# Kernel tuning notes

Measured on AMD Instinct MI355X. Metric: run time of the kernel, lower is better.

Reference implementation:

```python
import jax, jax.numpy as jnp
import numpy as np

N = 100000   # nodes
E = 1600000  # edges (avg degree 16)
D = 128      # in_channels == out_channels
L2_EPS = 1e-12   # F.normalize eps
GN_EPS = 1e-5    # GraphNorm eps


def setup_inputs() -> dict:
    key = jax.random.key(0)
    ks = jax.random.split(key, 6)
    x = jax.random.normal(ks[0], (N, D), dtype=jnp.float32)
    edge_index = jax.random.randint(ks[1], (2, E), 0, N, dtype=jnp.int32)
    batch = jnp.zeros((N,), dtype=jnp.int32)  # single graph
    scale = 1.0 / np.sqrt(D)
    Wl = jax.random.normal(ks[2], (D, D), dtype=jnp.float32) * scale  # SAGE lin_l (neighbor), has bias
    bl = jnp.zeros((D,), dtype=jnp.float32)
    Wr = jax.random.normal(ks[3], (D, D), dtype=jnp.float32) * scale  # SAGE lin_r (root), no bias
    gn_weight = jnp.ones((D,), dtype=jnp.float32)       # GraphNorm gamma
    gn_bias = jnp.zeros((D,), dtype=jnp.float32)        # GraphNorm beta
    gn_mean_scale = jnp.ones((D,), dtype=jnp.float32)   # GraphNorm alpha
    return {"x": x, "edge_index": edge_index, "batch": batch,
            "Wl": Wl, "bl": bl, "Wr": Wr,
            "gn_weight": gn_weight, "gn_bias": gn_bias, "gn_mean_scale": gn_mean_scale}


def reference(x, edge_index, batch, Wl, bl, Wr, gn_weight, gn_bias, gn_mean_scale):
    src, dst = edge_index[0], edge_index[1]
    n = x.shape[0]
    # ---- SAGEConv (aggr='mean', normalize=True) ----
    deg = jax.ops.segment_sum(jnp.ones(src.shape[0], x.dtype), dst, num_segments=n)
    agg = jax.ops.segment_sum(x[src], dst, num_segments=n)  # gather -> scatter-add [N, D]
    agg = agg / jnp.maximum(deg, 1.0)[:, None]              # mean aggregation
    h = agg @ Wl.T + bl + x @ Wr.T                          # lin_l(agg) + lin_r(x)
    h = h / jnp.maximum(jnp.linalg.norm(h, axis=-1, keepdims=True), L2_EPS)  # row L2 norm
    # ---- GraphNorm (batch is all zeros -> single graph stats) ----
    mean = jnp.mean(h, axis=0, keepdims=True)               # [1, D]
    centered = h - gn_mean_scale * mean
    var = jnp.mean(centered * centered, axis=0, keepdims=True)
    h = gn_weight * centered / jnp.sqrt(var + GN_EPS) + gn_bias
    # ---- activation (exact GELU, as torch nn.GELU) + dropout(eval=identity) + residual ----
    h = jax.nn.gelu(h, approximate=False)
    return h + x
```

## Files before the change

### kernel.cpp

```cpp
#include <hip/hip_runtime.h>
#include <cstdint>

#define DF 128

typedef float f32x4 __attribute__((ext_vector_type(4)));
typedef short bf16x8 __attribute__((ext_vector_type(8)));

__device__ __forceinline__ unsigned short f2bf(float f) {
  unsigned int u = __float_as_uint(f);
  return (unsigned short)((u + 0x7fffu + ((u >> 16) & 1u)) >> 16);
}
__device__ __forceinline__ unsigned int pack2(float lo, float hi) {
  return (unsigned int)f2bf(lo) | ((unsigned int)f2bf(hi) << 16);
}
__device__ __forceinline__ float bflo(unsigned int u) { return __uint_as_float(u << 16); }
__device__ __forceinline__ float bfhi(unsigned int u) { return __uint_as_float(u & 0xffff0000u); }

__global__ void k_wcvt(const float* __restrict__ Wl, const float* __restrict__ Wr,
                       unsigned short* __restrict__ wbf) {
  int i = blockIdx.x * 256 + threadIdx.x;
  int c = i >> 8;
  int k = i & 255;
  float v = (k < DF) ? Wl[c * DF + k] : Wr[c * DF + (k - DF)];
  wbf[i] = f2bf(v);
}

__global__ void k_xcvt(const float* __restrict__ x, unsigned int* __restrict__ xbf, int total8) {
  int i = blockIdx.x * 256 + threadIdx.x;
  if (i >= total8) return;
  const float4* xr = (const float4*)(x + (size_t)i * 8);
  float4 a = xr[0], b = xr[1];
  uint4 v;
  v.x = pack2(a.x, a.y);
  v.y = pack2(a.z, a.w);
  v.z = pack2(b.x, b.y);
  v.w = pack2(b.z, b.w);
  ((uint4*)xbf)[i] = v;
}

__global__ void k_deg(const int* __restrict__ ei, int* __restrict__ deg, int E) {
  int e = blockIdx.x * 256 + threadIdx.x;
  if (e < E) atomicAdd(&deg[ei[(size_t)E + e]], 1);
}

__global__ void k_off(const int* __restrict__ deg, int* __restrict__ start,
                      int* __restrict__ cursor, int* __restrict__ total, int n) {
  int i = blockIdx.x * 256 + threadIdx.x;
  if (i < n) {
    int d = deg[i];
    int p = atomicAdd(total, d);
    start[i] = p;
    cursor[i] = p;
  }
}

__global__ void k_fill(const int* __restrict__ ei, int* __restrict__ cursor,
                       int* __restrict__ adj, int E) {
  int e = blockIdx.x * 256 + threadIdx.x;
  if (e < E) {
    int s = ei[e];
    int t = ei[(size_t)E + e];
    int p = atomicAdd(&cursor[t], 1);
    adj[p] = s;
  }
}

template <int BF>
__global__ void k_agg(const float* __restrict__ xf, const unsigned int* __restrict__ xb,
                      const int* __restrict__ start, const int* __restrict__ deg,
                      const int* __restrict__ adj, unsigned short* __restrict__ aggbf, int n) {
  int node = blockIdx.x * 4 + (threadIdx.x >> 6);
  if (node >= n) return;
  int lane = threadIdx.x & 63;
  int rs = start[node];
  int d = deg[node];
  float s0 = 0.f, s1 = 0.f;
  int j = 0;
  for (; j + 4 <= d; j += 4) {
    int i0 = adj[rs + j], i1 = adj[rs + j + 1], i2 = adj[rs + j + 2], i3 = adj[rs + j + 3];
    if (BF) {
      unsigned int u0 = xb[(size_t)i0 * 64 + lane], u1 = xb[(size_t)i1 * 64 + lane],
                   u2 = xb[(size_t)i2 * 64 + lane], u3 = xb[(size_t)i3 * 64 + lane];
      s0 += bflo(u0) + bflo(u1) + bflo(u2) + bflo(u3);
      s1 += bfhi(u0) + bfhi(u1) + bfhi(u2) + bfhi(u3);
    } else {
      const float2* x2 = (const float2*)xf;
      float2 v0 = x2[(size_t)i0 * 64 + lane], v1 = x2[(size_t)i1 * 64 + lane],
             v2 = x2[(size_t)i2 * 64 + lane], v3 = x2[(size_t)i3 * 64 + lane];
      s0 += v0.x + v1.x + v2.x + v3.x;
      s1 += v0.y + v1.y + v2.y + v3.y;
    }
  }
  for (; j < d; ++j) {
    int i0 = adj[rs + j];
    if (BF) {
      unsigned int u0 = xb[(size_t)i0 * 64 + lane];
      s0 += bflo(u0);
      s1 += bfhi(u0);
    } else {
      const float2* x2 = (const float2*)xf;
      float2 v = x2[(size_t)i0 * 64 + lane];
      s0 += v.x;
      s1 += v.y;
    }
  }
  float inv = 1.0f / (float)(d > 1 ? d : 1);
  *(unsigned int*)(aggbf + (size_t)node * DF + lane * 2) = pack2(s0 * inv, s1 * inv);
}

template <int XBF>
__global__ __launch_bounds__(256) void k_gemm(
    const unsigned short* __restrict__ aggbf, const unsigned short* __restrict__ xbf,
    const float* __restrict__ x, const unsigned short* __restrict__ wbf,
    const float* __restrict__ bl, float* __restrict__ hout,
    float* __restrict__ pf, int n) {
  __shared__ __align__(16) unsigned short Abuf[64 * 128];
  __shared__ __align__(16) unsigned short Bbuf[128 * 128];
  int tid = threadIdx.x;
  int node0 = blockIdx.x * 64;
  int wv = tid >> 6, lane = tid & 63;
  int lo = lane & 15, hi = lane >> 4;

  f32x4 acc[8] = {};

  int arow = wv * 16 + lo;
  int abase = arow * 256 + hi * 16;
  int aswz = (arow & 7) << 4;

  for (int ph = 0; ph < 2; ++ph) {
    if (ph) __syncthreads();
    if (ph == 0 || XBF) {
      const unsigned short* src = ph == 0 ? aggbf : xbf;
#pragma unroll
      for (int it = 0; it < 4; ++it) {
        int id = it * 256 + tid;
        int row = id >> 4;
        int inner = (id & 15) * 16;
        uint4 v = make_uint4(0u, 0u, 0u, 0u);
        int gr = node0 + row;
        if (gr < n) v = *(const uint4*)(src + (size_t)gr * DF + inner / 2);
        *(uint4*)((char*)Abuf + ((row * 256 + inner) ^ ((row & 7) << 4))) = v;
      }
    } else {
#pragma unroll
      for (int it = 0; it < 4; ++it) {
        int id = it * 256 + tid;
        int row = id >> 4;
        int inner = (id & 15) * 16;
        int e0 = inner / 2;
        uint4 v = make_uint4(0u, 0u, 0u, 0u);
        int gr = node0 + row;
        if (gr < n) {
          const float4* xr = (const float4*)(x + (size_t)gr * DF + e0);
          float4 a = xr[0], b = xr[1];
          v.x = pack2(a.x, a.y);
          v.y = pack2(a.z, a.w);
          v.z = pack2(b.x, b.y);
          v.w = pack2(b.z, b.w);
        }
        *(uint4*)((char*)Abuf + ((row * 256 + inner) ^ ((row & 7) << 4))) = v;
      }
    }
#pragma unroll
    for (int it = 0; it < 8; ++it) {
      int id = it * 256 + tid;
      int c = id >> 4;
      int inner = (id & 15) * 16;
      uint4 v = *(const uint4*)((const char*)wbf + (size_t)c * 512 + ph * 256 + inner);
      *(uint4*)((char*)Bbuf + ((c * 256 + inner) ^ ((c & 7) << 4))) = v;
    }
    __syncthreads();
#pragma unroll
    for (int kk = 0; kk < 4; ++kk) {
      bf16x8 af = *(const bf16x8*)((const char*)Abuf + ((abase + kk * 64) ^ aswz));
#pragma unroll
      for (int f = 0; f < 8; ++f) {
        int brow = f * 16 + lo;
        int bb = (brow * 256 + hi * 16 + kk * 64) ^ ((brow & 7) << 4);
        bf16x8 bfr = *(const bf16x8*)((const char*)Bbuf + bb);
        acc[f] = __builtin_amdgcn_mfma_f32_16x16x32_bf16(af, bfr, acc[f], 0, 0, 0);
      }
    }
  }

  int r0 = node0 + wv * 16 + hi * 4;
#pragma unroll
  for (int f = 0; f < 8; ++f) {
    float b = bl[f * 16 + lo];
#pragma unroll
    for (int r = 0; r < 4; ++r) acc[f][r] += b;
  }
#pragma unroll
  for (int r = 0; r < 4; ++r) {
    if (r0 + r >= n) {
#pragma unroll
      for (int f = 0; f < 8; ++f) acc[f][r] = 0.f;
    }
  }
  float ss[4] = {0.f, 0.f, 0.f, 0.f};
#pragma unroll
  for (int f = 0; f < 8; ++f)
#pragma unroll
    for (int r = 0; r < 4; ++r) ss[r] += acc[f][r] * acc[f][r];
#pragma unroll
  for (int m = 1; m <= 8; m <<= 1) {
#pragma unroll
    for (int r = 0; r < 4; ++r) ss[r] += __shfl_xor(ss[r], m, 64);
  }
#pragma unroll
  for (int r = 0; r < 4; ++r) {
    float inv = 1.0f / fmaxf(sqrtf(ss[r]), 1e-12f);
#pragma unroll
    for (int f = 0; f < 8; ++f) acc[f][r] *= inv;
  }
  float s1[8], s2[8];
#pragma unroll
  for (int f = 0; f < 8; ++f) { s1[f] = 0.f; s2[f] = 0.f; }
#pragma unroll
  for (int f = 0; f < 8; ++f) {
#pragma unroll
    for (int r = 0; r < 4; ++r) {
      float v = acc[f][r];
      s1[f] += v;
      s2[f] += v * v;
      if (r0 + r < n) hout[(size_t)(r0 + r) * DF + f * 16 + lo] = v;
    }
  }
#pragma unroll
  for (int f = 0; f < 8; ++f) {
    s1[f] += __shfl_xor(s1[f], 16, 64);
    s1[f] += __shfl_xor(s1[f], 32, 64);
    s2[f] += __shfl_xor(s2[f], 16, 64);
    s2[f] += __shfl_xor(s2[f], 32, 64);
  }
  __syncthreads();
  float* red = (float*)Abuf;
  if (hi == 0) {
#pragma unroll
    for (int f = 0; f < 8; ++f) {
      red[wv * 256 + f * 16 + lo] = s1[f];
      red[wv * 256 + 128 + f * 16 + lo] = s2[f];
    }
  }
  __syncthreads();
  float v = red[tid] + red[256 + tid] + red[512 + tid] + red[768 + tid];
  pf[(size_t)blockIdx.x * 256 + tid] = v;
}

__global__ void k_reduce(const float* __restrict__ pf, float* __restrict__ pf2, int NB) {
  int g = blockIdx.x, t = threadIdx.x;
  int L = (NB + 15) / 16;
  int b0 = g * L, b1 = (b0 + L < NB) ? b0 + L : NB;
  float a = 0.f;
  for (int r = b0; r < b1; ++r) a += pf[(size_t)r * 256 + t];
  pf2[g * 256 + t] = a;
}

__global__ void k_coef(const float* __restrict__ pf2,
                       const float* __restrict__ gnw, const float* __restrict__ gnb,
                       const float* __restrict__ alpha, float* __restrict__ coef, int n) {
  int j = threadIdx.x;
  float s = 0.f, q = 0.f;
#pragma unroll
  for (int g = 0; g < 16; ++g) {
    s += pf2[g * 256 + j];
    q += pf2[g * 256 + 128 + j];
  }
  float invn = 1.0f / (float)n;
  float mean = s * invn;
  float m2 = q * invn;
  float a = alpha[j];
  float var = m2 - mean * mean * (2.0f * a - a * a);
  float ca = gnw[j] / sqrtf(var + 1e-5f);
  float cb = gnb[j] - ca * a * mean;
  coef[j] = ca;
  coef[DF + j] = cb;
}

__global__ void k_final(float* __restrict__ out, const float* __restrict__ x,
                        const float* __restrict__ coef, int total4) {
  int i = blockIdx.x * 256 + threadIdx.x;
  if (i >= total4) return;
  int cj = (i & 31) * 4;
  float4 h = ((const float4*)out)[i];
  float4 xv = ((const float4*)x)[i];
  float4 ca = *(const float4*)(coef + cj);
  float4 cb = *(const float4*)(coef + DF + cj);
  float4 o;
#define GEL(comp)                                                         \
  {                                                                       \
    float v = ca.comp * h.comp + cb.comp;                                 \
    float g = 0.5f * v * (1.0f + erff(v * 0.70710678118654752f));         \
    o.comp = g + xv.comp;                                                 \
  }
  GEL(x) GEL(y) GEL(z) GEL(w)
#undef GEL
  ((float4*)out)[i] = o;
}

extern "C" void kernel_launch(void* const* d_in, const int* in_sizes, int n_in,
                              void* d_out, int out_size, void* d_ws, size_t ws_size,
                              hipStream_t stream) {
  const float* x = (const float*)d_in[0];
  const int* ei = (const int*)d_in[1];
  const float* Wl = (const float*)d_in[3];
  const float* bl = (const float*)d_in[4];
  const float* Wr = (const float*)d_in[5];
  const float* gnw = (const float*)d_in[6];
  const float* gnb = (const float*)d_in[7];
  const float* alpha = (const float*)d_in[8];
  int n = in_sizes[2];
  int E = in_sizes[1] / 2;
  int NB = (n + 63) / 64;
  float* out = (float*)d_out;
  (void)n_in; (void)out_size;

  char* ws = (char*)d_ws;
  int* deg = (int*)ws;
  int* total = (int*)(ws + (size_t)n * 4);
  size_t zbytes = (size_t)(n + 1) * 4;
  size_t off = (zbytes + 255) & ~(size_t)255;
  auto carve = [&](size_t b) {
    char* p = ws + off;
    off = (off + b + 255) & ~(size_t)255;
    return p;
  };
  int* start = (int*)carve((size_t)n * 4);
  int* cursor = (int*)carve((size_t)n * 4);
  int* adjv = (int*)carve((size_t)E * 4);
  unsigned short* wbf = (unsigned short*)carve((size_t)DF * 256 * 2);
  float* coef = (float*)carve(256 * 4);
  float* pf = (float*)carve((size_t)NB * 256 * 4);
  float* pf2 = (float*)carve(16 * 256 * 4);
  unsigned short* aggbf = (unsigned short*)carve((size_t)n * DF * 2);
  size_t need_bf = off + (size_t)n * DF * 2;
  int useBF = (ws_size >= need_bf) ? 1 : 0;
  unsigned int* xbf = (unsigned int*)carve((size_t)n * DF * 2);

  hipMemsetAsync(ws, 0, zbytes, stream);
  k_wcvt<<<(DF * 256) / 256, 256, 0, stream>>>(Wl, Wr, wbf);
  k_deg<<<(E + 255) / 256, 256, 0, stream>>>(ei, deg, E);
  k_off<<<(n + 255) / 256, 256, 0, stream>>>(deg, start, cursor, total, n);
  k_fill<<<(E + 255) / 256, 256, 0, stream>>>(ei, cursor, adjv, E);
  if (useBF) {
    k_xcvt<<<(n * 16 + 255) / 256, 256, 0, stream>>>(x, xbf, n * 16);
    k_agg<1><<<(n + 3) / 4, 256, 0, stream>>>(x, xbf, start, deg, adjv, aggbf, n);
    k_gemm<1><<<NB, 256, 0, stream>>>(aggbf, (const unsigned short*)xbf, x, wbf, bl, out, pf, n);
  } else {
    k_agg<0><<<(n + 3) / 4, 256, 0, stream>>>(x, xbf, start, deg, adjv, aggbf, n);
    k_gemm<0><<<NB, 256, 0, stream>>>(aggbf, (const unsigned short*)xbf, x, wbf, bl, out, pf, n);
  }
  k_reduce<<<16, 256, 0, stream>>>(pf, pf2, NB);
  k_coef<<<1, DF, 0, stream>>>(pf2, gnw, gnb, alpha, coef, n);
  k_final<<<(n * (DF / 4) + 255) / 256, 256, 0, stream>>>(out, x, coef, n * (DF / 4));
}
```

Measured before the change: 470.7 us.

## Bucket edges by 64-node tile and fuse aggregation into GEMM via LDS atomics

Replaces the per-node CSR build (global atomics for degree, offset and fill) with a deterministic block histogram, scan and scatter that buckets edges by destination tile of 64 nodes, packing source and local destination into one word. The GEMM kernel then aggregates its tile's neighbours itself, accumulating in shared memory with float atomics, computing degrees locally, and writing bf16 A tiles straight to LDS. This removes the separate aggregation kernel and the global round trip of the aggregated matrix. In exchange it relies on heavy LDS atomic traffic and larger shared memory per block, which may lower occupancy. Summation order also becomes nondeterministic.

```diff
diff --git a/kernel.cpp b/kernel.cpp
--- a/kernel.cpp
+++ b/kernel.cpp
@@ -38,99 +38,205 @@
   ((uint4*)xbf)[i] = v;
 }
 
-__global__ void k_deg(const int* __restrict__ ei, int* __restrict__ deg, int E) {
-  int e = blockIdx.x * 256 + threadIdx.x;
-  if (e < E) atomicAdd(&deg[ei[(size_t)E + e]], 1);
-}
-
-__global__ void k_off(const int* __restrict__ deg, int* __restrict__ start,
-                      int* __restrict__ cursor, int* __restrict__ total, int n) {
-  int i = blockIdx.x * 256 + threadIdx.x;
-  if (i < n) {
-    int d = deg[i];
-    int p = atomicAdd(total, d);
-    start[i] = p;
-    cursor[i] = p;
-  }
-}
-
-__global__ void k_fill(const int* __restrict__ ei, int* __restrict__ cursor,
-                       int* __restrict__ adj, int E) {
-  int e = blockIdx.x * 256 + threadIdx.x;
-  if (e < E) {
-    int s = ei[e];
-    int t = ei[(size_t)E + e];
-    int p = atomicAdd(&cursor[t], 1);
-    adj[p] = s;
-  }
-}
-
-template <int BF>
-__global__ void k_agg(const float* __restrict__ xf, const unsigned int* __restrict__ xb,
-                      const int* __restrict__ start, const int* __restrict__ deg,
-                      const int* __restrict__ adj, unsigned short* __restrict__ aggbf, int n) {
-  int node = blockIdx.x * 4 + (threadIdx.x >> 6);
-  if (node >= n) return;
-  int lane = threadIdx.x & 63;
-  int rs = start[node];
-  int d = deg[node];
-  float s0 = 0.f, s1 = 0.f;
-  int j = 0;
-  for (; j + 4 <= d; j += 4) {
-    int i0 = adj[rs + j], i1 = adj[rs + j + 1], i2 = adj[rs + j + 2], i3 = adj[rs + j + 3];
-    if (BF) {
-      unsigned int u0 = xb[(size_t)i0 * 64 + lane], u1 = xb[(size_t)i1 * 64 + lane],
-                   u2 = xb[(size_t)i2 * 64 + lane], u3 = xb[(size_t)i3 * 64 + lane];
-      s0 += bflo(u0) + bflo(u1) + bflo(u2) + bflo(u3);
-      s1 += bfhi(u0) + bfhi(u1) + bfhi(u2) + bfhi(u3);
-    } else {
-      const float2* x2 = (const float2*)xf;
-      float2 v0 = x2[(size_t)i0 * 64 + lane], v1 = x2[(size_t)i1 * 64 + lane],
-             v2 = x2[(size_t)i2 * 64 + lane], v3 = x2[(size_t)i3 * 64 + lane];
-      s0 += v0.x + v1.x + v2.x + v3.x;
-      s1 += v0.y + v1.y + v2.y + v3.y;
-    }
-  }
-  for (; j < d; ++j) {
-    int i0 = adj[rs + j];
-    if (BF) {
-      unsigned int u0 = xb[(size_t)i0 * 64 + lane];
-      s0 += bflo(u0);
-      s1 += bfhi(u0);
-    } else {
-      const float2* x2 = (const float2*)xf;
-      float2 v = x2[(size_t)i0 * 64 + lane];
-      s0 += v.x;
-      s1 += v.y;
-    }
-  }
-  float inv = 1.0f / (float)(d > 1 ? d : 1);
-  *(unsigned int*)(aggbf + (size_t)node * DF + lane * 2) = pack2(s0 * inv, s1 * inv);
+__global__ __launch_bounds__(256) void k_hist(const int* __restrict__ ei,
+                                              unsigned int* __restrict__ hist,
+                                              int E, int NBK, int CE) {
+  __shared__ unsigned int h[4096];
+  for (int i = threadIdx.x; i < NBK; i += 256) h[i] = 0u;
+  __syncthreads();
+  int b0 = blockIdx.x * CE;
+  int b1 = b0 + CE < E ? b0 + CE : E;
+  for (int e = b0 + threadIdx.x; e < b1; e += 256)
+    atomicAdd(&h[((unsigned int)ei[(size_t)E + e]) >> 6], 1u);
+  __syncthreads();
+  for (int i = threadIdx.x; i < NBK; i += 256)
+    hist[(size_t)blockIdx.x * NBK + i] = h[i];
+}
+
+__global__ void k_btot(const unsigned int* __restrict__ hist, unsigned int* __restrict__ tot,
+                       int NBK, int NBLK) {
+  int j = blockIdx.x * 256 + threadIdx.x;
+  if (j >= NBK) return;
+  unsigned int s = 0u;
+  for (int b = 0; b < NBLK; ++b) s += hist[(size_t)b * NBK + j];
+  tot[j] = s;
+}
+
+__global__ __launch_bounds__(256) void k_scan(const unsigned int* __restrict__ tot,
+                                              unsigned int* __restrict__ bstart,
+                                              int NBK, int CHK) {
+  __shared__ unsigned int sums[256];
+  int t = threadIdx.x;
+  unsigned int loc[16];
+  unsigned int s = 0u;
+#pragma unroll
+  for (int k = 0; k < 16; ++k) {
+    if (k < CHK) {
+      int j = t * CHK + k;
+      loc[k] = s;
+      s += (j < NBK) ? tot[j] : 0u;
+    }
+  }
+  sums[t] = s;
+  __syncthreads();
+  for (int off = 1; off < 256; off <<= 1) {
+    unsigned int a = (t >= off) ? sums[t - off] : 0u;
+    __syncthreads();
+    sums[t] += a;
+    __syncthreads();
+  }
+  unsigned int basev = (t > 0) ? sums[t - 1] : 0u;
+#pragma unroll
+  for (int k = 0; k < 16; ++k) {
+    if (k < CHK) {
+      int j = t * CHK + k;
+      if (j < NBK) bstart[j] = basev + loc[k];
+    }
+  }
+  if (t == 255) bstart[NBK] = sums[255];
+}
+
+__global__ void k_base(const unsigned int* __restrict__ hist,
+                       const unsigned int* __restrict__ bstart,
+                       unsigned int* __restrict__ base, int NBK, int NBLK) {
+  int j = blockIdx.x * 256 + threadIdx.x;
+  if (j >= NBK) return;
+  unsigned int run = bstart[j];
+  for (int b = 0; b < NBLK; ++b) {
+    base[(size_t)b * NBK + j] = run;
+    run += hist[(size_t)b * NBK + j];
+  }
+}
+
+__global__ __launch_bounds__(256) void k_scat(const int* __restrict__ ei,
+                                              const unsigned int* __restrict__ base,
+                                              unsigned int* __restrict__ ebuf,
+                                              int E, int NBK, int CE) {
+  __shared__ unsigned int cur[4096];
+  for (int i = threadIdx.x; i < NBK; i += 256)
+    cur[i] = base[(size_t)blockIdx.x * NBK + i];
+  __syncthreads();
+  int b0 = blockIdx.x * CE;
+  int b1 = b0 + CE < E ? b0 + CE : E;
+  for (int e = b0 + threadIdx.x; e < b1; e += 256) {
+    unsigned int s = (unsigned int)ei[e];
+    unsigned int t = (unsigned int)ei[(size_t)E + e];
+    unsigned int p = atomicAdd(&cur[t >> 6], 1u);
+    ebuf[p] = (s << 6) | (t & 63u);
+  }
 }
 
 template <int XBF>
 __global__ __launch_bounds__(256) void k_gemm(
-    const unsigned short* __restrict__ aggbf, const unsigned short* __restrict__ xbf,
-    const float* __restrict__ x, const unsigned short* __restrict__ wbf,
-    const float* __restrict__ bl, float* __restrict__ hout,
-    float* __restrict__ pf, int n) {
-  __shared__ __align__(16) unsigned short Abuf[64 * 128];
-  __shared__ __align__(16) unsigned short Bbuf[128 * 128];
+    const unsigned int* __restrict__ ebuf, const unsigned int* __restrict__ bstart,
+    const unsigned int* __restrict__ xb, const float* __restrict__ x,
+    const unsigned short* __restrict__ wbf, const float* __restrict__ bl,
+    float* __restrict__ hout, float* __restrict__ pf, int n) {
+  __shared__ __align__(16) char smem[49408];
+  float* aggF = (float*)smem;
+  unsigned short* Bbuf = (unsigned short*)smem;
+  unsigned short* Abuf = (unsigned short*)(smem + 32768);
+  unsigned int* degS = (unsigned int*)(smem + 49152);
+  float* red = (float*)(smem + 32768);
+
   int tid = threadIdx.x;
   int node0 = blockIdx.x * 64;
   int wv = tid >> 6, lane = tid & 63;
   int lo = lane & 15, hi = lane >> 4;
 
+  {
+    float4 z = make_float4(0.f, 0.f, 0.f, 0.f);
+    float4* az = (float4*)aggF;
+    for (int i = tid; i < 2048; i += 256) az[i] = z;
+    if (tid < 64) degS[tid] = 0u;
+  }
+  __syncthreads();
+
+  int segStart = (int)bstart[blockIdx.x];
+  int L = (int)bstart[blockIdx.x + 1] - segStart;
+  int nfull = L >> 6;
+  const float2* x2 = (const float2*)x;
+  for (int c = wv; c < nfull; c += 4) {
+    int basee = segStart + (c << 6);
+    unsigned int ent = ebuf[basee + lane];
+    atomicAdd(&degS[ent & 63u], 1u);
+    for (int j0 = 0; j0 < 64; j0 += 8) {
+      int dl[8];
+      unsigned int rr[8];
+      float2 ff[8];
+#pragma unroll
+      for (int k2 = 0; k2 < 8; ++k2) {
+        unsigned int u = __shfl(ent, j0 + k2, 64);
+        dl[k2] = (int)(u & 63u);
+        if (XBF) rr[k2] = xb[(size_t)(u >> 6) * 64 + lane];
+        else ff[k2] = x2[(size_t)(u >> 6) * 64 + lane];
+      }
+#pragma unroll
+      for (int k2 = 0; k2 < 8; ++k2) {
+        float a0 = XBF ? bflo(rr[k2]) : ff[k2].x;
+        float a1 = XBF ? bfhi(rr[k2]) : ff[k2].y;
+        atomicAdd(&aggF[dl[k2] * 128 + lane * 2], a0);
+        atomicAdd(&aggF[dl[k2] * 128 + lane * 2 + 1], a1);
+      }
+    }
+  }
+  int trem = L & 63;
+  if (trem && wv == (nfull & 3)) {
+    int basee = segStart + (nfull << 6);
+    unsigned int ent = 0u;
+    if (lane < trem) {
+      ent = ebuf[basee + lane];
+      atomicAdd(&degS[ent & 63u], 1u);
+    }
+    for (int j0 = 0; j0 < trem; j0 += 8) {
+      int dl[8];
+      unsigned int rr[8];
+      float2 ff[8];
+#pragma unroll
+      for (int k2 = 0; k2 < 8; ++k2) {
+        if (j0 + k2 < trem) {
+          unsigned int u = __shfl(ent, j0 + k2, 64);
+          dl[k2] = (int)(u & 63u);
+          if (XBF) rr[k2] = xb[(size_t)(u >> 6) * 64 + lane];
+          else ff[k2] = x2[(size_t)(u >> 6) * 64 + lane];
+        }
+      }
+#pragma unroll
+      for (int k2 = 0; k2 < 8; ++k2) {
+        if (j0 + k2 < trem) {
+          float a0 = XBF ? bflo(rr[k2]) : ff[k2].x;
+          float a1 = XBF ? bfhi(rr[k2]) : ff[k2].y;
+          atomicAdd(&aggF[dl[k2] * 128 + lane * 2], a0);
+          atomicAdd(&aggF[dl[k2] * 128 + lane * 2 + 1], a1);
+        }
+      }
+    }
+  }
+  __syncthreads();
+
+  for (int c = tid; c < 1024; c += 256) {
+    int row = c >> 4;
+    int part = c & 15;
+    unsigned int d = degS[row];
+    float inv = 1.0f / (float)(d > 1u ? d : 1u);
+    const float* s = &aggF[row * 128 + part * 8];
+    uint4 v;
+    v.x = pack2(s[0] * inv, s[1] * inv);
+    v.y = pack2(s[2] * inv, s[3] * inv);
+    v.z = pack2(s[4] * inv, s[5] * inv);
+    v.w = pack2(s[6] * inv, s[7] * inv);
+    *(uint4*)((char*)Abuf + ((row * 256 + part * 16) ^ ((row & 7) << 4))) = v;
+  }
+  __syncthreads();
+
   f32x4 acc[8] = {};
-
   int arow = wv * 16 + lo;
   int abase = arow * 256 + hi * 16;
   int aswz = (arow & 7) << 4;
 
   for (int ph = 0; ph < 2; ++ph) {
-    if (ph) __syncthreads();
-    if (ph == 0 || XBF) {
-      const unsigned short* src = ph == 0 ? aggbf : xbf;
+    if (ph) {
+      __syncthreads();
 #pragma unroll
       for (int it = 0; it < 4; ++it) {
         int id = it * 256 + tid;
@@ -138,25 +244,17 @@
         int inner = (id & 15) * 16;
         uint4 v = make_uint4(0u, 0u, 0u, 0u);
         int gr = node0 + row;
-        if (gr < n) v = *(const uint4*)(src + (size_t)gr * DF + inner / 2);
-        *(uint4*)((char*)Abuf + ((row * 256 + inner) ^ ((row & 7) << 4))) = v;
-      }
-    } else {
-#pragma unroll
-      for (int it = 0; it < 4; ++it) {
-        int id = it * 256 + tid;
-        int row = id >> 4;
-        int inner = (id & 15) * 16;
-        int e0 = inner / 2;
-        uint4 v = make_uint4(0u, 0u, 0u, 0u);
-        int gr = node0 + row;
         if (gr < n) {
-          const float4* xr = (const float4*)(x + (size_t)gr * DF + e0);
-          float4 a = xr[0], b = xr[1];
-          v.x = pack2(a.x, a.y);
-          v.y = pack2(a.z, a.w);
-          v.z = pack2(b.x, b.y);
-          v.w = pack2(b.z, b.w);
+          if (XBF) {
+            v = *(const uint4*)((const unsigned short*)xb + (size_t)gr * DF + inner / 2);
+          } else {
+            const float4* xr = (const float4*)(x + (size_t)gr * DF + inner / 2);
+            float4 a = xr[0], b = xr[1];
+            v.x = pack2(a.x, a.y);
+            v.y = pack2(a.z, a.w);
+            v.z = pack2(b.x, b.y);
+            v.w = pack2(b.z, b.w);
+          }
         }
         *(uint4*)((char*)Abuf + ((row * 256 + inner) ^ ((row & 7) << 4))) = v;
       }
@@ -164,10 +262,10 @@
 #pragma unroll
     for (int it = 0; it < 8; ++it) {
       int id = it * 256 + tid;
-      int c = id >> 4;
+      int cC = id >> 4;
       int inner = (id & 15) * 16;
-      uint4 v = *(const uint4*)((const char*)wbf + (size_t)c * 512 + ph * 256 + inner);
-      *(uint4*)((char*)Bbuf + ((c * 256 + inner) ^ ((c & 7) << 4))) = v;
+      uint4 v = *(const uint4*)((const char*)wbf + (size_t)cC * 512 + ph * 256 + inner);
+      *(uint4*)((char*)Bbuf + ((cC * 256 + inner) ^ ((cC & 7) << 4))) = v;
     }
     __syncthreads();
 #pragma unroll
@@ -234,7 +332,6 @@
     s2[f] += __shfl_xor(s2[f], 32, 64);
   }
   __syncthreads();
-  float* red = (float*)Abuf;
   if (hi == 0) {
 #pragma unroll
     for (int f = 0; f < 8; ++f) {
@@ -311,46 +408,46 @@
   const float* alpha = (const float*)d_in[8];
   int n = in_sizes[2];
   int E = in_sizes[1] / 2;
-  int NB = (n + 63) / 64;
+  int NBK = (n + 63) / 64;
+  const int NBLK = 128;
+  int CE = (E + NBLK - 1) / NBLK;
+  int CHK = (NBK + 255) / 256;
   float* out = (float*)d_out;
   (void)n_in; (void)out_size;
 
   char* ws = (char*)d_ws;
-  int* deg = (int*)ws;
-  int* total = (int*)(ws + (size_t)n * 4);
-  size_t zbytes = (size_t)(n + 1) * 4;
-  size_t off = (zbytes + 255) & ~(size_t)255;
+  size_t off = 0;
   auto carve = [&](size_t b) {
     char* p = ws + off;
     off = (off + b + 255) & ~(size_t)255;
     return p;
   };
-  int* start = (int*)carve((size_t)n * 4);
-  int* cursor = (int*)carve((size_t)n * 4);
-  int* adjv = (int*)carve((size_t)E * 4);
+  unsigned int* ebuf = (unsigned int*)carve((size_t)E * 4);
+  unsigned int* hist = (unsigned int*)carve((size_t)NBLK * NBK * 4);
+  unsigned int* base = (unsigned int*)carve((size_t)NBLK * NBK * 4);
+  unsigned int* tot = (unsigned int*)carve((size_t)NBK * 4);
+  unsigned int* bstart = (unsigned int*)carve((size_t)(NBK + 1) * 4);
   unsigned short* wbf = (unsigned short*)carve((size_t)DF * 256 * 2);
   float* coef = (float*)carve(256 * 4);
-  float* pf = (float*)carve((size_t)NB * 256 * 4);
+  float* pf = (float*)carve((size_t)NBK * 256 * 4);
   float* pf2 = (float*)carve(16 * 256 * 4);
-  unsigned short* aggbf = (unsigned short*)carve((size_t)n * DF * 2);
   size_t need_bf = off + (size_t)n * DF * 2;
   int useBF = (ws_size >= need_bf) ? 1 : 0;
   unsigned int* xbf = (unsigned int*)carve((size_t)n * DF * 2);
 
-  hipMemsetAsync(ws, 0, zbytes, stream);
   k_wcvt<<<(DF * 256) / 256, 256, 0, stream>>>(Wl, Wr, wbf);
-  k_deg<<<(E + 255) / 256, 256, 0, stream>>>(ei, deg, E);
-  k_off<<<(n + 255) / 256, 256, 0, stream>>>(deg, start, cursor, total, n);
-  k_fill<<<(E + 255) / 256, 256, 0, stream>>>(ei, cursor, adjv, E);
+  k_hist<<<NBLK, 256, 0, stream>>>(ei, hist, E, NBK, CE);
+  k_btot<<<(NBK + 255) / 256, 256, 0, stream>>>(hist, tot, NBK, NBLK);
+  k_scan<<<1, 256, 0, stream>>>(tot, bstart, NBK, CHK);
+  k_base<<<(NBK + 255) / 256, 256, 0, stream>>>(hist, bstart, base, NBK, NBLK);
+  k_scat<<<NBLK, 256, 0, stream>>>(ei, base, ebuf, E, NBK, CE);
   if (useBF) {
     k_xcvt<<<(n * 16 + 255) / 256, 256, 0, stream>>>(x, xbf, n * 16);
-    k_agg<1><<<(n + 3) / 4, 256, 0, stream>>>(x, xbf, start, deg, adjv, aggbf, n);
-    k_gemm<1><<<NB, 256, 0, stream>>>(aggbf, (const unsigned short*)xbf, x, wbf, bl, out, pf, n);
+    k_gemm<1><<<NBK, 256, 0, stream>>>(ebuf, bstart, xbf, x, wbf, bl, out, pf, n);
   } else {
-    k_agg<0><<<(n + 3) / 4, 256, 0, stream>>>(x, xbf, start, deg, adjv, aggbf, n);
-    k_gemm<0><<<NB, 256, 0, stream>>>(aggbf, (const unsigned short*)xbf, x, wbf, bl, out, pf, n);
-  }
-  k_reduce<<<16, 256, 0, stream>>>(pf, pf2, NB);
+    k_gemm<0><<<NBK, 256, 0, stream>>>(ebuf, bstart, xbf, x, wbf, bl, out, pf, n);
+  }
+  k_reduce<<<16, 256, 0, stream>>>(pf, pf2, NBK);
   k_coef<<<1, DF, 0, stream>>>(pf2, gnw, gnb, alpha, coef, n);
-  k_final<<<(n * (DF / 4) + 255) / 256, 256, 0, stream>>>(out, x, coef, n * (DF / 4));
-}
+  k_final<<<(n * 32 + 255) / 256, 256, 0, stream>>>(out, x, coef, n * 32);
+}
```

New measurement: 1.473 ms. 3.13x slower.
